# Kernel tuning notes

Hardware: AMD Instinct MI355X
Metric: run time of the kernel (lower is better)

The kernel has to match this reference:

```python
import jax, jax.numpy as jnp
import numpy as np

TAU = 2.0         # LIFNode default tau
VTH = 1.0         # v_threshold
ALPHA = 2.0       # ATan surrogate alpha
TIME_STEP = 4     # hard-coded in RecurrentLIFNode
NUM_LAYERS = 4
HIDDEN = 512
INPUT = 512
T, B = 128, 512

@jax.custom_vjp
def atan_spike(x):
    # heaviside forward, ATan surrogate backward (spikingjelly surrogate.ATan)
    return (x >= 0.0).astype(x.dtype)

def _atan_fwd(x):
    return atan_spike(x), x

def _atan_bwd(x, g):
    return (g * (ALPHA / 2.0) / (1.0 + (jnp.pi / 2.0 * ALPHA * x) ** 2),)

atan_spike.defvjp(_atan_fwd, _atan_bwd)

def lif_burst(v, inp):
    # run one LIFCell time_step times with fixed input `inp`, accumulate averages
    acc_v = jnp.zeros_like(v)
    acc_s = jnp.zeros_like(v)
    for _ in range(TIME_STEP):
        v = v + (inp - v) / TAU          # neuronal_charge (decay_input=True, v_reset=None)
        s = atan_spike(v - VTH)          # neuronal_fire
        v = v - s * VTH                  # soft reset (v_reset=None)
        acc_v = acc_v + v
        acc_s = acc_s + s
    return v, acc_v / TIME_STEP, acc_s / TIME_STEP


def setup_inputs() -> dict:
    key = jax.random.key(0)
    k1, k2, k3 = jax.random.split(key, 3)
    x = jax.random.normal(k1, (T, B, INPUT), dtype=jnp.float32)
    bound = 1.0 / np.sqrt(INPUT)
    W = jax.random.uniform(k2, (HIDDEN, INPUT), dtype=jnp.float32, minval=-bound, maxval=bound)
    b = jax.random.uniform(k3, (HIDDEN,), dtype=jnp.float32, minval=-bound, maxval=bound)
    return {"x": x, "W": W, "b": b}


def reference(x, W, b):
    # x: [T, B, input]; project once (linear_ih)
    xp = jnp.einsum('tbi,hi->tbh', x, W) + b   # [T, B, H]
    Bsz, H = x.shape[1], W.shape[0]
    init_state = jnp.zeros((NUM_LAYERS, Bsz, H), dtype=x.dtype)  # current_state persists across t

    def step(cur, xt):
        curs = [cur[i] for i in range(NUM_LAYERS)]
        y = xt
        new_vs = []
        last_spk = None
        for i in range(NUM_LAYERS):
            curs[i], avg_v, avg_s = lif_burst(curs[i], y)
            new_vs.append(avg_v)
            y = avg_v          # next layer consumes averaged membrane state
            last_spk = avg_s
        return jnp.stack(curs), (last_spk, jnp.stack(new_vs))

    _, (out, states_seq) = jax.lax.scan(step, init_state, xp)
    # out: [T, B, H] averaged spikes of last layer; final new_states_list: [L, B, H]
    return out, states_seq[-1]
```

## Files before the change

### kernel.cpp

```cpp
#include <hip/hip_runtime.h>
#include <stdint.h>

#define TT 128
#define BSZ 512
#define HID 512
#define KDIM 512
#define BH (BSZ*HID)

typedef float v2f __attribute__((ext_vector_type(2)));

__global__ __launch_bounds__(256, 1) void gemm_f32(
    const float* __restrict__ A, const float* __restrict__ W,
    const float* __restrict__ bias, float* __restrict__ C) {
  __shared__ float As[2][16][132];
  __shared__ float Bs[2][16][260];
  const int t  = threadIdx.x;
  const int m0 = blockIdx.y * 128;
  const int n0 = blockIdx.x * 256;
  const int tx = t & 15;
  const int ty = t >> 4;
  const int r0 = t >> 2;
  const int kg = t & 3;

  v2f acc[8][8];
  #pragma unroll
  for (int i = 0; i < 8; ++i)
    #pragma unroll
    for (int j = 0; j < 8; ++j) acc[i][j] = (v2f){0.f, 0.f};

  const float* Ap = A + (size_t)(m0 + r0) * KDIM + kg * 4;
  const float* Wp = W + (size_t)(n0 + r0) * KDIM + kg * 4;

  float4 a0 = *(const float4*)Ap;
  float4 a1 = *(const float4*)(Ap + (size_t)64  * KDIM);
  float4 w0 = *(const float4*)Wp;
  float4 w1 = *(const float4*)(Wp + (size_t)64  * KDIM);
  float4 w2 = *(const float4*)(Wp + (size_t)128 * KDIM);
  float4 w3 = *(const float4*)(Wp + (size_t)192 * KDIM);

  #define STAGE(BUF) do { \
    As[BUF][kg*4+0][r0]     = a0.x; As[BUF][kg*4+1][r0]     = a0.y; \
    As[BUF][kg*4+2][r0]     = a0.z; As[BUF][kg*4+3][r0]     = a0.w; \
    As[BUF][kg*4+0][r0+64]  = a1.x; As[BUF][kg*4+1][r0+64]  = a1.y; \
    As[BUF][kg*4+2][r0+64]  = a1.z; As[BUF][kg*4+3][r0+64]  = a1.w; \
    Bs[BUF][kg*4+0][r0]     = w0.x; Bs[BUF][kg*4+1][r0]     = w0.y; \
    Bs[BUF][kg*4+2][r0]     = w0.z; Bs[BUF][kg*4+3][r0]     = w0.w; \
    Bs[BUF][kg*4+0][r0+64]  = w1.x; Bs[BUF][kg*4+1][r0+64]  = w1.y; \
    Bs[BUF][kg*4+2][r0+64]  = w1.z; Bs[BUF][kg*4+3][r0+64]  = w1.w; \
    Bs[BUF][kg*4+0][r0+128] = w2.x; Bs[BUF][kg*4+1][r0+128] = w2.y; \
    Bs[BUF][kg*4+2][r0+128] = w2.z; Bs[BUF][kg*4+3][r0+128] = w2.w; \
    Bs[BUF][kg*4+0][r0+192] = w3.x; Bs[BUF][kg*4+1][r0+192] = w3.y; \
    Bs[BUF][kg*4+2][r0+192] = w3.z; Bs[BUF][kg*4+3][r0+192] = w3.w; \
  } while (0)

  STAGE(0);

  int cur = 0;
  for (int k0 = 0; k0 < KDIM; k0 += 16) {
    __syncthreads();
    const bool more = (k0 + 16 < KDIM);
    if (more) {
      a0 = *(const float4*)(Ap + k0 + 16);
      a1 = *(const float4*)(Ap + (size_t)64  * KDIM + k0 + 16);
      w0 = *(const float4*)(Wp + k0 + 16);
      w1 = *(const float4*)(Wp + (size_t)64  * KDIM + k0 + 16);
      w2 = *(const float4*)(Wp + (size_t)128 * KDIM + k0 + 16);
      w3 = *(const float4*)(Wp + (size_t)192 * KDIM + k0 + 16);
    }

    #pragma unroll
    for (int kk = 0; kk < 16; ++kk) {
      const float4 xa0 = *(const float4*)&As[cur][kk][ty*8];
      const float4 xa1 = *(const float4*)&As[cur][kk][ty*8 + 4];
      const float a[8] = {xa0.x,xa0.y,xa0.z,xa0.w,xa1.x,xa1.y,xa1.z,xa1.w};
      v2f ad[8];
      #pragma unroll
      for (int i = 0; i < 8; ++i) ad[i] = (v2f){a[i], a[i]};
      #pragma unroll
      for (int q = 0; q < 4; ++q) {
        const float4 xb = *(const float4*)&Bs[cur][kk][64*q + tx*4];
        const v2f b0 = (v2f){xb.x, xb.y};
        const v2f b1 = (v2f){xb.z, xb.w};
        #pragma unroll
        for (int i = 0; i < 8; ++i) {
          acc[i][2*q]   = __builtin_elementwise_fma(ad[i], b0, acc[i][2*q]);
          acc[i][2*q+1] = __builtin_elementwise_fma(ad[i], b1, acc[i][2*q+1]);
        }
      }
    }

    if (more) {
      const int nb = cur ^ 1;
      STAGE(nb);
    }
    cur ^= 1;
  }
  #undef STAGE

  float4 bv[4];
  #pragma unroll
  for (int q = 0; q < 4; ++q) bv[q] = *(const float4*)&bias[n0 + 64*q + tx*4];
  #pragma unroll
  for (int i = 0; i < 8; ++i) {
    float* cp = C + (size_t)(m0 + ty*8 + i) * HID + n0 + tx*4;
    #pragma unroll
    for (int q = 0; q < 4; ++q) {
      const float4 v = {acc[i][2*q].x + bv[q].x, acc[i][2*q].y + bv[q].y,
                        acc[i][2*q+1].x + bv[q].z, acc[i][2*q+1].y + bv[q].w};
      *(float4*)(cp + 64*q) = v;
    }
  }
}

__device__ __forceinline__ float lif_step(float y, float v[4], float av[4]) {
  float as3 = 0.f;
  #pragma unroll
  for (int l = 0; l < 4; ++l) {
    float vv = v[l];
    float accv = 0.f, accs = 0.f;
    #pragma unroll
    for (int k = 0; k < 4; ++k) {
      const float d = y - vv;
      vv = __builtin_fmaf(d, 0.5f, vv);
      const float spk = (vv >= 1.0f) ? 1.0f : 0.0f;
      vv -= spk;
      accv += vv;
      accs += spk;
    }
    v[l] = vv;
    const float a = accv * 0.25f;
    av[l] = a;
    y = a;
    as3 = accs;
  }
  return as3;
}

__global__ __launch_bounds__(256) void lif_scan(
    const float* __restrict__ xp, float* __restrict__ outp, float* __restrict__ vstate,
    int tc, int first, int last) {
  const int idx = blockIdx.x * 256 + threadIdx.x;
  float v[4];
  if (first) {
    #pragma unroll
    for (int l = 0; l < 4; ++l) v[l] = 0.f;
  } else {
    #pragma unroll
    for (int l = 0; l < 4; ++l) v[l] = vstate[(size_t)l * BH + idx];
  }
  float av[4] = {0.f, 0.f, 0.f, 0.f};
  const float* p = xp + idx;
  float* op = outp + idx;

  if ((tc & 7) == 0 && tc >= 16) {
    float curb[8];
    #pragma unroll
    for (int i = 0; i < 8; ++i) curb[i] = __builtin_nontemporal_load(&p[(size_t)i * BH]);
    for (int t = 0; t + 8 < tc; t += 8) {
      float nxtb[8];
      #pragma unroll
      for (int i = 0; i < 8; ++i)
        nxtb[i] = __builtin_nontemporal_load(&p[(size_t)(i + 8) * BH]);
      #pragma unroll
      for (int i = 0; i < 8; ++i) {
        const float as3 = lif_step(curb[i], v, av);
        __builtin_nontemporal_store(as3 * 0.25f, &op[(size_t)i * BH]);
      }
      #pragma unroll
      for (int i = 0; i < 8; ++i) curb[i] = nxtb[i];
      p += 8 * BH; op += 8 * BH;
    }
    #pragma unroll
    for (int i = 0; i < 8; ++i) {
      const float as3 = lif_step(curb[i], v, av);
      __builtin_nontemporal_store(as3 * 0.25f, &op[(size_t)i * BH]);
    }
  } else {
    for (int t = 0; t < tc; ++t) {
      const float as3 = lif_step(p[0], v, av);
      *op = as3 * 0.25f;
      p += BH; op += BH;
    }
  }

  if (last) {
    #pragma unroll
    for (int l = 0; l < 4; ++l) vstate[(size_t)l * BH + idx] = av[l];
  } else {
    #pragma unroll
    for (int l = 0; l < 4; ++l) vstate[(size_t)l * BH + idx] = v[l];
  }
}

extern "C" void kernel_launch(void* const* d_in, const int* in_sizes, int n_in,
                              void* d_out, int out_size, void* d_ws, size_t ws_size,
                              hipStream_t stream) {
  const float* x = (const float*)d_in[0];
  const float* W = (const float*)d_in[1];
  const float* b = (const float*)d_in[2];
  float* out    = (float*)d_out;
  float* states = out + (size_t)TT * BH;

  int tc = TT;
  while (tc > 1 && (size_t)tc * BH * 4ull > ws_size) tc >>= 1;
  float* xp = (float*)d_ws;
  const int nc = TT / tc;

  for (int c = 0; c < nc; ++c) {
    hipLaunchKernelGGL(gemm_f32, dim3(HID / 256, tc * BSZ / 128), dim3(256), 0, stream,
                       x + (size_t)c * tc * BH, W, b, xp);
    hipLaunchKernelGGL(lif_scan, dim3(BH / 256), dim3(256), 0, stream,
                       xp, out + (size_t)c * tc * BH, states,
                       tc, c == 0 ? 1 : 0, c == nc - 1 ? 1 : 0);
  }
}
```

Baseline: 594.8 us.

## Restructure GEMM tiling: smaller M tile, A rows loaded per-wave from global

The fp32 projection GEMM now uses a 32x256 output tile per block instead of 128x256. Each wave owns 8 rows and reads its A values straight from global memory as wave-uniform loads, so A is no longer staged through shared memory. Each thread keeps an 8x4 accumulator instead of 8x8 paired vectors. The smaller footprint allows four blocks per CU and four times as many blocks. The cost is less reuse of W per block, so W is reloaded from L2 more often, and the packed v2f FMA form is dropped in favour of scalar FMAs.

```diff
diff --git a/kernel.cpp b/kernel.cpp
--- a/kernel.cpp
+++ b/kernel.cpp
@@ -7,42 +7,33 @@
 #define KDIM 512
 #define BH (BSZ*HID)
 
-typedef float v2f __attribute__((ext_vector_type(2)));
-
-__global__ __launch_bounds__(256, 1) void gemm_f32(
+__global__ __launch_bounds__(256, 4) void gemm_f32(
     const float* __restrict__ A, const float* __restrict__ W,
     const float* __restrict__ bias, float* __restrict__ C) {
-  __shared__ float As[2][16][132];
   __shared__ float Bs[2][16][260];
-  const int t  = threadIdx.x;
-  const int m0 = blockIdx.y * 128;
-  const int n0 = blockIdx.x * 256;
-  const int tx = t & 15;
-  const int ty = t >> 4;
-  const int r0 = t >> 2;
-  const int kg = t & 3;
+  const int t    = threadIdx.x;
+  const int m0   = blockIdx.y * 32;
+  const int n0   = blockIdx.x * 256;
+  const int lane = t & 63;
+  const int wid  = __builtin_amdgcn_readfirstlane(t >> 6);
+  const int r0   = t >> 2;
+  const int kg   = t & 3;
 
-  v2f acc[8][8];
+  float acc[8][4];
   #pragma unroll
   for (int i = 0; i < 8; ++i)
     #pragma unroll
-    for (int j = 0; j < 8; ++j) acc[i][j] = (v2f){0.f, 0.f};
+    for (int j = 0; j < 4; ++j) acc[i][j] = 0.f;
 
-  const float* Ap = A + (size_t)(m0 + r0) * KDIM + kg * 4;
   const float* Wp = W + (size_t)(n0 + r0) * KDIM + kg * 4;
+  const float* Aw = A + (size_t)(m0 + wid * 8) * KDIM;
 
-  float4 a0 = *(const float4*)Ap;
-  float4 a1 = *(const float4*)(Ap + (size_t)64  * KDIM);
   float4 w0 = *(const float4*)Wp;
   float4 w1 = *(const float4*)(Wp + (size_t)64  * KDIM);
   float4 w2 = *(const float4*)(Wp + (size_t)128 * KDIM);
   float4 w3 = *(const float4*)(Wp + (size_t)192 * KDIM);
 
   #define STAGE(BUF) do { \
-    As[BUF][kg*4+0][r0]     = a0.x; As[BUF][kg*4+1][r0]     = a0.y; \
-    As[BUF][kg*4+2][r0]     = a0.z; As[BUF][kg*4+3][r0]     = a0.w; \
-    As[BUF][kg*4+0][r0+64]  = a1.x; As[BUF][kg*4+1][r0+64]  = a1.y; \
-    As[BUF][kg*4+2][r0+64]  = a1.z; As[BUF][kg*4+3][r0+64]  = a1.w; \
     Bs[BUF][kg*4+0][r0]     = w0.x; Bs[BUF][kg*4+1][r0]     = w0.y; \
     Bs[BUF][kg*4+2][r0]     = w0.z; Bs[BUF][kg*4+3][r0]     = w0.w; \
     Bs[BUF][kg*4+0][r0+64]  = w1.x; Bs[BUF][kg*4+1][r0+64]  = w1.y; \
@@ -60,8 +51,6 @@
     __syncthreads();
     const bool more = (k0 + 16 < KDIM);
     if (more) {
-      a0 = *(const float4*)(Ap + k0 + 16);
-      a1 = *(const float4*)(Ap + (size_t)64  * KDIM + k0 + 16);
       w0 = *(const float4*)(Wp + k0 + 16);
       w1 = *(const float4*)(Wp + (size_t)64  * KDIM + k0 + 16);
       w2 = *(const float4*)(Wp + (size_t)128 * KDIM + k0 + 16);
@@ -69,22 +58,22 @@
     }
 
     #pragma unroll
-    for (int kk = 0; kk < 16; ++kk) {
-      const float4 xa0 = *(const float4*)&As[cur][kk][ty*8];
-      const float4 xa1 = *(const float4*)&As[cur][kk][ty*8 + 4];
-      const float a[8] = {xa0.x,xa0.y,xa0.z,xa0.w,xa1.x,xa1.y,xa1.z,xa1.w};
-      v2f ad[8];
+    for (int kq = 0; kq < 4; ++kq) {
+      float4 aq[8];
       #pragma unroll
-      for (int i = 0; i < 8; ++i) ad[i] = (v2f){a[i], a[i]};
+      for (int i = 0; i < 8; ++i)
+        aq[i] = *(const float4*)(Aw + (size_t)i * KDIM + k0 + kq * 4);
       #pragma unroll
-      for (int q = 0; q < 4; ++q) {
-        const float4 xb = *(const float4*)&Bs[cur][kk][64*q + tx*4];
-        const v2f b0 = (v2f){xb.x, xb.y};
-        const v2f b1 = (v2f){xb.z, xb.w};
+      for (int kk = 0; kk < 4; ++kk) {
+        const float4 xb = *(const float4*)&Bs[cur][kq*4 + kk][lane*4];
         #pragma unroll
         for (int i = 0; i < 8; ++i) {
-          acc[i][2*q]   = __builtin_elementwise_fma(ad[i], b0, acc[i][2*q]);
-          acc[i][2*q+1] = __builtin_elementwise_fma(ad[i], b1, acc[i][2*q+1]);
+          const float ai = (kk == 0) ? aq[i].x : (kk == 1) ? aq[i].y
+                         : (kk == 2) ? aq[i].z : aq[i].w;
+          acc[i][0] = __builtin_fmaf(ai, xb.x, acc[i][0]);
+          acc[i][1] = __builtin_fmaf(ai, xb.y, acc[i][1]);
+          acc[i][2] = __builtin_fmaf(ai, xb.z, acc[i][2]);
+          acc[i][3] = __builtin_fmaf(ai, xb.w, acc[i][3]);
         }
       }
     }
@@ -97,18 +86,12 @@
   }
   #undef STAGE
 
-  float4 bv[4];
-  #pragma unroll
-  for (int q = 0; q < 4; ++q) bv[q] = *(const float4*)&bias[n0 + 64*q + tx*4];
+  const float4 bv = *(const float4*)&bias[n0 + lane*4];
   #pragma unroll
   for (int i = 0; i < 8; ++i) {
-    float* cp = C + (size_t)(m0 + ty*8 + i) * HID + n0 + tx*4;
-    #pragma unroll
-    for (int q = 0; q < 4; ++q) {
-      const float4 v = {acc[i][2*q].x + bv[q].x, acc[i][2*q].y + bv[q].y,
-                        acc[i][2*q+1].x + bv[q].z, acc[i][2*q+1].y + bv[q].w};
-      *(float4*)(cp + 64*q) = v;
-    }
+    const float4 v = {acc[i][0] + bv.x, acc[i][1] + bv.y,
+                      acc[i][2] + bv.z, acc[i][3] + bv.w};
+    *(float4*)(C + (size_t)(m0 + wid*8 + i) * HID + n0 + lane*4) = v;
   }
 }
 
@@ -207,7 +190,7 @@
   const int nc = TT / tc;
 
   for (int c = 0; c < nc; ++c) {
-    hipLaunchKernelGGL(gemm_f32, dim3(HID / 256, tc * BSZ / 128), dim3(256), 0, stream,
+    hipLaunchKernelGGL(gemm_f32, dim3(HID / 256, tc * BSZ / 32), dim3(256), 0, stream,
                        x + (size_t)c * tc * BH, W, b, xp);
     hipLaunchKernelGGL(lif_scan, dim3(BH / 256), dim3(256), 0, stream,
                        xp, out + (size_t)c * tc * BH, states,
```

Result: slower. 618.1 us (+3.9%).
